# Performance work log

Hardware: AMD Instinct MI355X
Metric: run time of the kernel (lower is better)

## Reference

```python
import jax, jax.numpy as jnp
import numpy as np

B, T, H, O = 256, 512, 1024, 256


def setup_inputs() -> dict:
    key = jax.random.key(0)
    k0, k1, k2, k3, k4 = jax.random.split(key, 5)
    scale_ih = 1.0 / np.sqrt(1 + H)
    scale_ho = 1.0 / np.sqrt(H)
    return {
        "x": jax.random.normal(k0, (B, T), dtype=jnp.float32),
        "W_ih": jax.random.normal(k1, (1 + H, H), dtype=jnp.float32) * scale_ih,
        "b_ih": jax.random.normal(k2, (H,), dtype=jnp.float32) * scale_ih,
        "W_ho": jax.random.normal(k3, (H, O), dtype=jnp.float32) * scale_ho,
        "b_ho": jax.random.normal(k4, (O,), dtype=jnp.float32) * scale_ho,
    }


def reference(x, W_ih, b_ih, W_ho, b_ho):
    # Elman RNN cell: hidden = tanh(W_ih @ [x_t; h]); output = W_ho @ h_T.
    # Only the final timestep's output is returned by the original module,
    # so h2o is applied once to the final hidden state (identical math).
    batch = x.shape[0]
    h0 = jnp.zeros((batch, W_ih.shape[1]), dtype=x.dtype)

    def step(h, x_t):  # x_t: [B], h: [B, H]
        combined = jnp.concatenate([x_t[:, None], h], axis=1)  # [B, 1+H]
        h_new = jnp.tanh(combined @ W_ih + b_ih)               # [B, H]
        return h_new, None

    h_final, _ = jax.lax.scan(step, h0, x.T)  # scan over T
    return h_final @ W_ho + b_ho              # [B, O]
```

## Files before the change

kernel.cpp:

```cpp
#include <hip/hip_runtime.h>
#include <hip/hip_bf16.h>


#define Bsz 256
#define Tn  512
#define Hn  1024
#define On  256

typedef __attribute__((ext_vector_type(8))) _Float16 f16x8;
typedef __attribute__((ext_vector_type(4))) float f32x4;
typedef __attribute__((ext_vector_type(4))) int   i32x4;
typedef __attribute__((ext_vector_type(2))) int   i32x2;

__device__ __forceinline__ unsigned f2h(float f) {
    _Float16 h = (_Float16)f;
    union { _Float16 h; unsigned short s; } u; u.h = h;
    return (unsigned)u.s;
}

__device__ __forceinline__ f16x8 as_f16x8(i32x4 v) {
    union { i32x4 i; f16x8 h; } u; u.i = v; return u.h;
}

__device__ __forceinline__ float fast_tanh(float x) {
    float xc = fminf(fmaxf(x, -9.f), 9.f);
    float e  = __builtin_amdgcn_exp2f(xc * 2.8853900817779268f);
    return (e - 1.f) * __builtin_amdgcn_rcpf(e + 1.f);
}

__device__ __forceinline__ void stage_h_poll(const short* __restrict__ hsrc,
                                             short* __restrict__ htile,
                                             int row0, int w, int lane,
                                             unsigned tag) {
    const short* gp = hsrc + (size_t)(row0 + 2 * w) * Hn + lane * 8;
    i32x4 t0, t1, t2, t3;
    for (;;) {
        asm volatile(
            "global_load_dwordx4 %0, %4, off sc0 sc1\n\t"
            "global_load_dwordx4 %1, %4, off offset:1024 sc0 sc1\n\t"
            "global_load_dwordx4 %2, %4, off offset:2048 sc0 sc1\n\t"
            "global_load_dwordx4 %3, %4, off offset:3072 sc0 sc1\n\t"
            "s_waitcnt vmcnt(0)"
            : "=&v"(t0), "=&v"(t1), "=&v"(t2), "=&v"(t3)
            : "v"(gp) : "memory");
        unsigned bad = 0;
#pragma unroll
        for (int e = 0; e < 4; ++e)
            bad |= (unsigned)(t0[e] ^ tag) | (unsigned)(t1[e] ^ tag) |
                   (unsigned)(t2[e] ^ tag) | (unsigned)(t3[e] ^ tag);
        if (!__any(bad & 1u)) break;
    }
    i32x4 tv[4] = {t0, t1, t2, t3};
#pragma unroll
    for (int k = 0; k < 4; ++k) {
        int row = 2 * w + (k >> 1);
        int g   = (k & 1) * 64 + lane;
        int idx = row * 128 + (g ^ (row & 7));
        *(i32x4*)(htile + idx * 8) = tv[k];
    }
}

#define MFMA_F16 __builtin_amdgcn_mfma_f32_16x16x32_f16

__global__ __launch_bounds__(512, 2) void rnn_kernel(
    const float* __restrict__ x,
    const float* __restrict__ W_ih,
    const float* __restrict__ b_ih,
    const float* __restrict__ W_ho,
    const float* __restrict__ b_ho,
    float* __restrict__ out,
    short* __restrict__ hbuf)
{
    const int tid  = threadIdx.x;
    const int lane = tid & 63;
    const int w    = tid >> 6;
    const int cg   = w >> 2;
    const int kq   = w & 3;
    const int q    = lane >> 4;
    const int n    = lane & 15;

    const int i = blockIdx.x & 15;
    const int j = blockIdx.x >> 4;
    const int colbase = j * 128 + cg * 64;
    const int owncol  = colbase + kq * 16 + 4 * q;
    const int row0    = i * 16;

    __shared__ float x_lds[16][Tn + 1];
    __shared__ short htile[16 * Hn];
    __shared__ float redbuf[8 * 3 * 272];

    for (int idx = tid; idx < 16 * Tn; idx += 512) {
        int r = idx >> 9, tt = idx & (Tn - 1);
        x_lds[r][tt] = x[(row0 + r) * Tn + tt];
    }

    f16x8 wfrag[32];
#pragma unroll
    for (int mt = 0; mt < 4; ++mt)
#pragma unroll
        for (int ks = 0; ks < 8; ++ks) {
#pragma unroll
            for (int e = 0; e < 8; ++e) {
                int k = kq * 256 + ks * 32 + q * 8 + e;
                wfrag[mt * 8 + ks][e] =
                    (_Float16)W_ih[(size_t)(1 + k) * Hn + colbase + mt * 16 + n];
            }
        }
    const float4 bias4 = *(const float4*)(b_ih + owncol);
    const float4 w04   = *(const float4*)(W_ih + owncol);

    __syncthreads();

    short* h0 = hbuf;
    short* h1 = hbuf + Bsz * Hn;
    const int swn   = n & 7;
    const int gbase = kq * 32;
    const f32x4 zero4 = {0.f, 0.f, 0.f, 0.f};

    for (int t = 0; t < Tn; ++t) {
        const float xv = x_lds[n][t];
        f32x4 aown = {bias4.x + xv * w04.x, bias4.y + xv * w04.y,
                      bias4.z + xv * w04.z, bias4.w + xv * w04.w};
        f32x4 hv;

        if (t > 0) {
            stage_h_poll((t & 1) ? h1 : h0, htile, row0, w, lane,
                         (unsigned)((t + 1) >> 1) & 1u);
            __syncthreads();

            f32x4 acc0 = (kq == 0) ? aown : zero4;
            f32x4 acc1 = (kq == 1) ? aown : zero4;
            f32x4 acc2 = (kq == 2) ? aown : zero4;
            f32x4 acc3 = (kq == 3) ? aown : zero4;
            const i32x4* lrow = (const i32x4*)(htile + n * Hn);
#pragma unroll
            for (int ks = 0; ks < 8; ++ks) {
                f16x8 b = as_f16x8(lrow[(gbase + ks * 4 + q) ^ swn]);
                acc0 = MFMA_F16(wfrag[0 * 8 + ks], b, acc0, 0, 0, 0);
                acc1 = MFMA_F16(wfrag[1 * 8 + ks], b, acc1, 0, 0, 0);
                acc2 = MFMA_F16(wfrag[2 * 8 + ks], b, acc2, 0, 0, 0);
                acc3 = MFMA_F16(wfrag[3 * 8 + ks], b, acc3, 0, 0, 0);
            }

#define WRITE_PART(MT, ACC)                                                  \
            if (kq != MT) {                                                  \
                int src = (kq < MT) ? kq : kq - 1;                           \
                float* bp = redbuf + ((cg * 4 + MT) * 3 + src) * 272 + n;    \
                bp[(4 * q + 0) * 17] = ACC[0];                               \
                bp[(4 * q + 1) * 17] = ACC[1];                               \
                bp[(4 * q + 2) * 17] = ACC[2];                               \
                bp[(4 * q + 3) * 17] = ACC[3];                               \
            }
            WRITE_PART(0, acc0)
            WRITE_PART(1, acc1)
            WRITE_PART(2, acc2)
            WRITE_PART(3, acc3)
#undef WRITE_PART
            __syncthreads();

            hv = (kq == 0) ? acc0 : (kq == 1) ? acc1 : (kq == 2) ? acc2 : acc3;
            const float* bp = redbuf + (cg * 4 + kq) * 3 * 272 + n;
#pragma unroll
            for (int src = 0; src < 3; ++src) {
#pragma unroll
                for (int r = 0; r < 4; ++r)
                    hv[r] += bp[src * 272 + (4 * q + r) * 17];
            }
        } else {
            hv = aown;
        }

        unsigned tagn = (unsigned)((t + 2) >> 1) & 1u;
        unsigned e0 = f2h(fast_tanh(hv[0])), e1 = f2h(fast_tanh(hv[1]));
        unsigned e2 = f2h(fast_tanh(hv[2])), e3 = f2h(fast_tanh(hv[3]));
        i32x2 pk;
        pk[0] = (int)(((e0 & ~1u) | tagn) | (e1 << 16));
        pk[1] = (int)(((e2 & ~1u) | tagn) | (e3 << 16));
        short* hdst = (((t + 1) & 1) ? h1 : h0) + (size_t)(row0 + n) * Hn + owncol;
        asm volatile("global_store_dwordx2 %0, %1, off sc0 sc1"
                     :: "v"(hdst), "v"(pk) : "memory");
    }

    stage_h_poll(h0, htile, row0, w, lane, 0u);
    __syncthreads();

    f32x4 e0 = zero4, e1 = zero4;
    {
        const i32x4* lrow = (const i32x4*)(htile + n * Hn);
#pragma unroll
        for (int kk = 0; kk < 4; ++kk) {
            f16x8 af = as_f16x8(lrow[(w * 16 + kk * 4 + q) ^ swn]);
            f16x8 b0, b1;
#pragma unroll
            for (int e = 0; e < 8; ++e) {
                const float* wp = W_ho +
                    (size_t)(w * 128 + kk * 32 + q * 8 + e) * On + j * 32 + n;
                b0[e] = (_Float16)wp[0];
                b1[e] = (_Float16)wp[16];
            }
            e0 = MFMA_F16(af, b0, e0, 0, 0, 0);
            e1 = MFMA_F16(af, b1, e1, 0, 0, 0);
        }
    }
    {
        float* re = redbuf + w * 528;
#pragma unroll
        for (int r = 0; r < 4; ++r) {
            re[(4 * q + r) * 33 + n]      = e0[r];
            re[(4 * q + r) * 33 + 16 + n] = e1[r];
        }
    }
    __syncthreads();
    {
        int r = tid >> 5, c = tid & 31;
        float s = b_ho[j * 32 + c];
#pragma unroll
        for (int w8 = 0; w8 < 8; ++w8)
            s += redbuf[w8 * 528 + r * 33 + c];
        out[(size_t)(row0 + r) * On + j * 32 + c] = s;
    }
}

extern "C" void kernel_launch(void* const* d_in, const int* in_sizes, int n_in,
                              void* d_out, int out_size, void* d_ws, size_t ws_size,
                              hipStream_t stream) {
    const float* x    = (const float*)d_in[0];
    const float* W_ih = (const float*)d_in[1];
    const float* b_ih = (const float*)d_in[2];
    const float* W_ho = (const float*)d_in[3];
    const float* b_ho = (const float*)d_in[4];
    float* out = (float*)d_out;

    size_t need = (size_t)2 * Bsz * Hn * sizeof(short);
    if (ws_size < need) return;

    short* hbuf = (short*)d_ws;

    rnn_kernel<<<128, 512, 0, stream>>>(x, W_ih, b_ih, W_ho, b_ho, out, hbuf);
}
```

Measured before the change: 1.117 ms.

## Replace per-step block barrier with pairwise wave flags and vectorize partial-sum reduction

Each wave now stages only the K-quarter of the hidden tile that its own MFMAs consume, split across the two column-group waves that share that quarter. The block-wide __syncthreads after staging is replaced by an LDS atomic counter that each wave pair spins on, so a wave waits only for its partner. The reduction buffer is double-buffered by step parity and laid out for 128-bit vector writes and reads, replacing the padded scalar accesses. The spin-wait adds LDS atomic traffic and relies on the remaining reduction barrier to keep the staged tile safe from being overwritten while it is still being read.

```diff
diff --git a/kernel.cpp b/kernel.cpp
--- a/kernel.cpp
+++ b/kernel.cpp
@@ -28,21 +28,28 @@
     return (e - 1.f) * __builtin_amdgcn_rcpf(e + 1.f);
 }
 
-__device__ __forceinline__ void stage_h_poll(const short* __restrict__ hsrc,
-                                             short* __restrict__ htile,
-                                             int row0, int w, int lane,
-                                             unsigned tag) {
-    const short* gp = hsrc + (size_t)(row0 + 2 * w) * Hn + lane * 8;
+#define MFMA_F16 __builtin_amdgcn_mfma_f32_16x16x32_f16
+
+__device__ __forceinline__ void stage_quarter(const short* __restrict__ hsrc,
+                                              short* __restrict__ htile,
+                                              int row0, int cg, int kq,
+                                              int lane, unsigned tag) {
+    const int half = lane >> 5, gl = lane & 31, r0 = cg * 8;
+    const short* a0 = hsrc + (size_t)(row0 + r0 + 0 + half) * Hn + kq * 256 + gl * 8;
+    const short* a1 = hsrc + (size_t)(row0 + r0 + 2 + half) * Hn + kq * 256 + gl * 8;
+    const short* a2 = hsrc + (size_t)(row0 + r0 + 4 + half) * Hn + kq * 256 + gl * 8;
+    const short* a3 = hsrc + (size_t)(row0 + r0 + 6 + half) * Hn + kq * 256 + gl * 8;
     i32x4 t0, t1, t2, t3;
     for (;;) {
-        asm volatile(
-            "global_load_dwordx4 %0, %4, off sc0 sc1\n\t"
-            "global_load_dwordx4 %1, %4, off offset:1024 sc0 sc1\n\t"
-            "global_load_dwordx4 %2, %4, off offset:2048 sc0 sc1\n\t"
-            "global_load_dwordx4 %3, %4, off offset:3072 sc0 sc1\n\t"
-            "s_waitcnt vmcnt(0)"
-            : "=&v"(t0), "=&v"(t1), "=&v"(t2), "=&v"(t3)
-            : "v"(gp) : "memory");
+        asm volatile("global_load_dwordx4 %0, %1, off sc0 sc1"
+                     : "=&v"(t0) : "v"(a0) : "memory");
+        asm volatile("global_load_dwordx4 %0, %1, off sc0 sc1"
+                     : "=&v"(t1) : "v"(a1) : "memory");
+        asm volatile("global_load_dwordx4 %0, %1, off sc0 sc1"
+                     : "=&v"(t2) : "v"(a2) : "memory");
+        asm volatile("global_load_dwordx4 %0, %1, off sc0 sc1"
+                     : "=&v"(t3) : "v"(a3) : "memory");
+        asm volatile("s_waitcnt vmcnt(0)" ::: "memory");
         unsigned bad = 0;
 #pragma unroll
         for (int e = 0; e < 4; ++e)
@@ -52,15 +59,13 @@
     }
     i32x4 tv[4] = {t0, t1, t2, t3};
 #pragma unroll
-    for (int k = 0; k < 4; ++k) {
-        int row = 2 * w + (k >> 1);
-        int g   = (k & 1) * 64 + lane;
+    for (int p = 0; p < 4; ++p) {
+        int row = r0 + 2 * p + half;
+        int g   = kq * 32 + gl;
         int idx = row * 128 + (g ^ (row & 7));
-        *(i32x4*)(htile + idx * 8) = tv[k];
-    }
-}
-
-#define MFMA_F16 __builtin_amdgcn_mfma_f32_16x16x32_f16
+        *(i32x4*)(htile + idx * 8) = tv[p];
+    }
+}
 
 __global__ __launch_bounds__(512, 2) void rnn_kernel(
     const float* __restrict__ x,
@@ -87,7 +92,10 @@
 
     __shared__ float x_lds[16][Tn + 1];
     __shared__ short htile[16 * Hn];
-    __shared__ float redbuf[8 * 3 * 272];
+    __shared__ float redbuf[2][8 * 3 * 256];
+    __shared__ int   pairflag[4];
+
+    if (tid < 4) pairflag[tid] = 0;
 
     for (int idx = tid; idx < 16 * Tn; idx += 512) {
         int r = idx >> 9, tt = idx & (Tn - 1);
@@ -115,6 +123,7 @@
     short* h1 = hbuf + Bsz * Hn;
     const int swn   = n & 7;
     const int gbase = kq * 32;
+    const int slot  = (q * 16 + n) * 4;
     const f32x4 zero4 = {0.f, 0.f, 0.f, 0.f};
 
     for (int t = 0; t < Tn; ++t) {
@@ -124,9 +133,15 @@
         f32x4 hv;
 
         if (t > 0) {
-            stage_h_poll((t & 1) ? h1 : h0, htile, row0, w, lane,
-                         (unsigned)((t + 1) >> 1) & 1u);
-            __syncthreads();
+            stage_quarter((t & 1) ? h1 : h0, htile, row0, cg, kq, lane,
+                          (unsigned)((t + 1) >> 1) & 1u);
+            asm volatile("s_waitcnt lgkmcnt(0)" ::: "memory");
+            if (lane == 0)
+                __hip_atomic_fetch_add(&pairflag[kq], 1, __ATOMIC_RELAXED,
+                                       __HIP_MEMORY_SCOPE_WORKGROUP);
+            while (__hip_atomic_load(&pairflag[kq], __ATOMIC_RELAXED,
+                                     __HIP_MEMORY_SCOPE_WORKGROUP) < 2 * t) {}
+            asm volatile("" ::: "memory");
 
             f32x4 acc0 = (kq == 0) ? aown : zero4;
             f32x4 acc1 = (kq == 1) ? aown : zero4;
@@ -142,14 +157,11 @@
                 acc3 = MFMA_F16(wfrag[3 * 8 + ks], b, acc3, 0, 0, 0);
             }
 
+            float* rb = redbuf[t & 1];
 #define WRITE_PART(MT, ACC)                                                  \
             if (kq != MT) {                                                  \
                 int src = (kq < MT) ? kq : kq - 1;                           \
-                float* bp = redbuf + ((cg * 4 + MT) * 3 + src) * 272 + n;    \
-                bp[(4 * q + 0) * 17] = ACC[0];                               \
-                bp[(4 * q + 1) * 17] = ACC[1];                               \
-                bp[(4 * q + 2) * 17] = ACC[2];                               \
-                bp[(4 * q + 3) * 17] = ACC[3];                               \
+                *(f32x4*)(rb + ((cg * 4 + MT) * 3 + src) * 256 + slot) = ACC;\
             }
             WRITE_PART(0, acc0)
             WRITE_PART(1, acc1)
@@ -159,13 +171,11 @@
             __syncthreads();
 
             hv = (kq == 0) ? acc0 : (kq == 1) ? acc1 : (kq == 2) ? acc2 : acc3;
-            const float* bp = redbuf + (cg * 4 + kq) * 3 * 272 + n;
-#pragma unroll
-            for (int src = 0; src < 3; ++src) {
-#pragma unroll
-                for (int r = 0; r < 4; ++r)
-                    hv[r] += bp[src * 272 + (4 * q + r) * 17];
-            }
+            const float* bp = rb + (cg * 4 + kq) * 3 * 256 + slot;
+            f32x4 p0 = *(const f32x4*)(bp);
+            f32x4 p1 = *(const f32x4*)(bp + 256);
+            f32x4 p2 = *(const f32x4*)(bp + 512);
+            hv = hv + p0 + p1 + p2;
         } else {
             hv = aown;
         }
@@ -181,7 +191,7 @@
                      :: "v"(hdst), "v"(pk) : "memory");
     }
 
-    stage_h_poll(h0, htile, row0, w, lane, 0u);
+    stage_quarter(h0, htile, row0, cg, kq, lane, 0u);
     __syncthreads();
 
     f32x4 e0 = zero4, e1 = zero4;
@@ -203,7 +213,7 @@
         }
     }
     {
-        float* re = redbuf + w * 528;
+        float* re = redbuf[0] + w * 528;
 #pragma unroll
         for (int r = 0; r < 4; ++r) {
             re[(4 * q + r) * 33 + n]      = e0[r];
@@ -216,7 +226,7 @@
         float s = b_ho[j * 32 + c];
 #pragma unroll
         for (int w8 = 0; w8 < 8; ++w8)
-            s += redbuf[w8 * 528 + r * 33 + c];
+            s += redbuf[0][w8 * 528 + r * 33 + c];
         out[(size_t)(row0 + r) * On + j * 32 + c] = s;
     }
 }
```

Result: faster. 1.082 ms (-3.2%).
